# Optimization experiments

Measured on AMD Instinct MI355X. Metric: run time of the kernel, lower is better.

The kernel has to match this reference:

```python
import jax, jax.numpy as jnp
import numpy as np

M = 41
RHO = M / 2.0          # rho=-1 -> M/2
OVERLAPS = 40

def _get_index():
    S = [(n1, n2)
         for n1 in range(-(M // 2), M // 2)
         for n2 in range(-(M // 2), M // 2)
         if abs(n1 * n2) <= RHO * (M // 2)]
    return np.asarray(S, dtype=np.int32)  # [K,2], K=1600 for defaults

_PAIRS = _get_index()


def setup_inputs() -> dict:
    key = jax.random.key(0)
    ks = jax.random.split(key, 7)
    B, L, N = 2, 2048, 2
    K = _PAIRS.shape[0]
    return {
        "x_real": jax.random.normal(ks[0], (B, L, N), jnp.float32),
        "x_imag": jax.random.normal(ks[1], (B, L, N), jnp.float32),
        "task_info": jax.random.uniform(ks[2], (B, 4), jnp.float32),
        "fc_wr": jax.random.normal(ks[3], (K,), jnp.float32) * 0.02,
        "fc_wi": jax.random.normal(ks[4], (K,), jnp.float32) * 0.02,
        "fc_br": jax.random.normal(ks[5], (1,), jnp.float32) * 0.02,
        "fc_bi": jax.random.normal(ks[6], (1,), jnp.float32) * 0.02,
    }


def reference(x_real, x_imag, task_info, fc_wr, fc_wi, fc_br, fc_bi):
    B, L, N = x_real.shape
    x0 = x_real + 1j * x_imag                      # [B,L,N] complex64
    # get_power: dBm -> Watts per mode
    P = 1e-3 * jnp.power(10.0, task_info[:, 0] / 10.0) / N   # [B]

    xf = jnp.fft.fft(x0, axis=1)                   # [B,L,N]
    idx = jnp.arange(L)
    n1 = jnp.asarray(_PAIRS[:, 0])
    n2 = jnp.asarray(_PAIRS[:, 1])

    # torch.roll(x, s, dim=1)[i] == x[(i - s) % L]; vectorize over all K pairs
    def gather(s):                                  # s: [K]
        return xf[:, (idx[:, None] - s[None, :]) % L, :]   # [B,L,K,N]

    A = gather(n1) * jnp.conj(gather(n1 + n2))      # [B,L,K,N]
    E = (A + jnp.roll(A, 1, axis=-1)) * gather(n2)  # [B,L,K,N]

    w = fc_wr + 1j * fc_wi                          # [K]
    b = fc_br[0] + 1j * fc_bi[0]
    delta = jnp.einsum('blkn,k->bln', E, w) + b     # ComplexLinear K->1
    delta = jnp.fft.ifft(delta, axis=1)

    out = (x0 + delta * P[:, None, None])[:, OVERLAPS // 2 : L - OVERLAPS // 2, :]
    # return real/imag stacked so the baseline output is real-valued
    return jnp.stack([out.real, out.imag], axis=-1)  # [B, L-OVERLAPS, N, 2]
```

## Files before the change

### kernel.cpp

```cpp
#include <hip/hip_runtime.h>


#define L_FFT 2048
#define NB 2
#define NM 2
#define ND 40
#define CROP 20
#define LOUT 2008

__device__ __forceinline__ float2 cmul(float2 a, float2 b) {
    return make_float2(a.x*b.x - a.y*b.y, a.x*b.y + a.y*b.x);
}
__device__ __forceinline__ float2 cmulc(float2 a, float2 b) {
    return make_float2(a.x*b.x + a.y*b.y, a.y*b.x - a.x*b.y);
}

template<int SIGN>
__device__ void build_tw(float2* tw, int tid) {
    if (tid < 512) {
        float ang = (float)(SIGN * tid) * 3.0679615757712823e-03f;
        tw[tid] = make_float2(__cosf(ang), __sinf(ang));
    }
}

template<int SIGN>
__device__ float2* fft2048_r4(float2* bufA, float2* bufB, const float2* tw, int tid) {
    float2* src = bufA;
    float2* dst = bufB;
    #pragma unroll
    for (int m = 1; m <= 256; m *= 4) {
        __syncthreads();
        int k2 = tid & (m - 1);
        int jm = tid - k2;
        float2 A = src[tid];
        float2 C = src[tid + 512];
        float2 B = src[tid + 1024];
        float2 D = src[tid + 1536];
        float2 T0 = make_float2(A.x + B.x, A.y + B.y);
        float2 T1 = make_float2(A.x - B.x, A.y - B.y);
        float2 T2 = make_float2(C.x + D.x, C.y + D.y);
        float2 cd = make_float2(C.x - D.x, C.y - D.y);
        float2 T3 = (SIGN < 0) ? make_float2(cd.y, -cd.x)
                               : make_float2(-cd.y, cd.x);
        float2 w1 = tw[jm];
        float2 w2 = cmul(w1, w1);
        float2 w3 = cmul(w2, w1);
        int base = 4 * jm + k2;
        dst[base]         = make_float2(T0.x + T2.x, T0.y + T2.y);
        dst[base + m]     = cmul(make_float2(T1.x + T3.x, T1.y + T3.y), w1);
        dst[base + 2*m]   = cmul(make_float2(T0.x - T2.x, T0.y - T2.y), w2);
        dst[base + 3*m]   = cmul(make_float2(T1.x - T3.x, T1.y - T3.y), w3);
        float2* t = src; src = dst; dst = t;
    }
    __syncthreads();
    #pragma unroll
    for (int it = 0; it < 2; ++it) {
        int q = tid + it * 512;
        float2 a = src[q];
        float2 b = src[q + 1024];
        dst[q]        = make_float2(a.x + b.x, a.y + b.y);
        dst[q + 1024] = make_float2(a.x - b.x, a.y - b.y);
    }
    float2* res = dst;
    __syncthreads();
    return res;
}

__global__ __launch_bounds__(512) void fft_fwd_kernel(const float* __restrict__ xr,
                                                      const float* __restrict__ xi,
                                                      float2* __restrict__ xf,
                                                      float* __restrict__ df) {
    __shared__ float2 bufA[L_FFT];
    __shared__ float2 bufB[L_FFT];
    __shared__ float2 tw[512];
    int bn = blockIdx.x;
    int b = bn >> 1, n = bn & 1;
    int tid = threadIdx.x;
    #pragma unroll
    for (int i = 0; i < 8; ++i)
        df[bn * (L_FFT * 2) + tid + i * 512] = 0.f;
    #pragma unroll
    for (int it = 0; it < 4; ++it) {
        int t = tid + it * 512;
        int gi = (b * L_FFT + t) * NM + n;
        bufA[t] = make_float2(xr[gi], xi[gi]);
    }
    build_tw<-1>(tw, tid);
    float2* res = fft2048_r4<-1>(bufA, bufB, tw, tid);
    #pragma unroll
    for (int it = 0; it < 4; ++it) {
        int f = tid + it * 512;
        xf[bn * L_FFT + f] = res[f];
    }
}

__global__ __launch_bounds__(256) void gs2_kernel(const float2* __restrict__ xf,
                                                  const float* __restrict__ wr,
                                                  const float* __restrict__ wi,
                                                  float* __restrict__ df) {
    __shared__ float2 xs0[336], xs1[336];
    __shared__ float2 Gs[296];
    __shared__ float wrs[40][4], wis[40][4];
    int blk = blockIdx.x;
    int b   = blk / 80;
    int rem = blk % 80;
    int dq  = rem >> 3;
    int l0  = (rem & 7) << 8;
    int tid = threadIdx.x;
    const float2* x0 = xf + (b * 2 + 0) * L_FFT;
    const float2* x1 = xf + (b * 2 + 1) * L_FFT;
    for (int i = tid; i < 336; i += 256) {
        int m = (l0 - 39 + i) & (L_FFT - 1);
        xs0[i] = x0[m];
        xs1[i] = x1[m];
    }
    if (tid < 160) {
        int n1i = tid >> 2, di = tid & 3;
        wrs[n1i][di] = wr[n1i * ND + dq * 4 + di];
        wis[n1i][di] = wi[n1i * ND + dq * 4 + di];
    }
    __syncthreads();
    float2 a0 = make_float2(0.f, 0.f);
    float2 a1 = make_float2(0.f, 0.f);
    #pragma unroll
    for (int di = 0; di < 4; ++di) {
        int d  = dq * 4 + di;
        int dd = d - 20;
        for (int j = tid; j < 295; j += 256) {
            float2 g0 = cmulc(xs0[j + 20], xs0[j + 20 - dd]);
            float2 g1 = cmulc(xs1[j + 20], xs1[j + 20 - dd]);
            Gs[j] = make_float2(g0.x + g1.x, g0.y + g1.y);
        }
        __syncthreads();
        float2 acc = make_float2(0.f, 0.f);
        #pragma unroll
        for (int n1i = 0; n1i < ND; ++n1i) {
            float2 g = Gs[tid + 39 - n1i];
            float wxr = wrs[n1i][di], wxi = wis[n1i][di];
            acc.x += wxr * g.x - wxi * g.y;
            acc.y += wxr * g.y + wxi * g.x;
        }
        int xvi = tid + 39 - dd;
        float2 c0 = cmul(acc, xs0[xvi]);
        float2 c1 = cmul(acc, xs1[xvi]);
        a0.x += c0.x; a0.y += c0.y;
        a1.x += c1.x; a1.y += c1.y;
        __syncthreads();
    }
    int base = (b * 2) * (L_FFT * 2) + (l0 + tid) * 2;
    unsafeAtomicAdd(&df[base + 0], a0.x);
    unsafeAtomicAdd(&df[base + 1], a0.y);
    unsafeAtomicAdd(&df[base + L_FFT * 2 + 0], a1.x);
    unsafeAtomicAdd(&df[base + L_FFT * 2 + 1], a1.y);
}

__global__ __launch_bounds__(512) void ifft_out_kernel(const float* __restrict__ df,
                                                       const float* __restrict__ xr,
                                                       const float* __restrict__ xi,
                                                       const float* __restrict__ task,
                                                       float* __restrict__ out) {
    __shared__ float2 bufA[L_FFT];
    __shared__ float2 bufB[L_FFT];
    __shared__ float2 tw[512];
    int bn = blockIdx.x;
    int b = bn >> 1, n = bn & 1;
    int tid = threadIdx.x;
    const float2* dfreq = (const float2*)df + bn * L_FFT;
    #pragma unroll
    for (int it = 0; it < 4; ++it)
        bufA[tid + it * 512] = dfreq[tid + it * 512];
    build_tw<1>(tw, tid);
    float2* res = fft2048_r4<1>(bufA, bufB, tw, tid);
    float P = 1e-3f * __powf(10.f, task[b * 4] * 0.1f) * 0.5f;
    float scale = P * (1.0f / (float)L_FFT);
    for (int t = CROP + tid; t < L_FFT - CROP; t += 512) {
        int gi = (b * L_FFT + t) * NM + n;
        float2 dv = res[t];
        int oi = ((b * LOUT + (t - CROP)) * NM + n) * 2;
        out[oi]     = xr[gi] + dv.x * scale;
        out[oi + 1] = xi[gi] + dv.y * scale;
    }
}

extern "C" void kernel_launch(void* const* d_in, const int* in_sizes, int n_in,
                              void* d_out, int out_size, void* d_ws, size_t ws_size,
                              hipStream_t stream) {
    const float* xr   = (const float*)d_in[0];
    const float* xi   = (const float*)d_in[1];
    const float* task = (const float*)d_in[2];
    const float* wr   = (const float*)d_in[3];
    const float* wi   = (const float*)d_in[4];
    float* out = (float*)d_out;

    float2* ws = (float2*)d_ws;
    float2* xf = ws;
    float*  df = (float*)(ws + 8192);

    hipLaunchKernelGGL(fft_fwd_kernel,  dim3(NB * NM), dim3(512), 0, stream, xr, xi, xf, df);
    hipLaunchKernelGGL(gs2_kernel,      dim3(160), dim3(256), 0, stream, xf, wr, wi, df);
    hipLaunchKernelGGL(ifft_out_kernel, dim3(NB * NM), dim3(512), 0, stream, df, xr, xi, task, out);
}
```

Baseline: 23.01 us.

## Fuse FFT, correlation and IFFT stages into one kernel with global-counter barriers

Replaces three kernel launches with a single persistent kernel of 80 blocks. Blocks synchronize through agent-scope atomic counters and spin-waits instead of kernel boundaries. The correlation stage now uses 512-thread blocks covering 512 output positions each, where it previously used 160 blocks of 256. The zeroing of df and the counters moves to a hipMemsetAsync. This removes two launch gaps but adds spin-wait overhead, and it relies on all 80 blocks being co-resident.

```diff
diff --git a/kernel.cpp b/kernel.cpp
--- a/kernel.cpp
+++ b/kernel.cpp
@@ -7,12 +7,28 @@
 #define ND 40
 #define CROP 20
 #define LOUT 2008
+#define NBLK 80
+#define NT 512
+#define SLAB 591
+#define GSZ 551
 
 __device__ __forceinline__ float2 cmul(float2 a, float2 b) {
     return make_float2(a.x*b.x - a.y*b.y, a.x*b.y + a.y*b.x);
 }
 __device__ __forceinline__ float2 cmulc(float2 a, float2 b) {
     return make_float2(a.x*b.x + a.y*b.y, a.y*b.x - a.x*b.y);
+}
+
+__device__ __forceinline__ void agent_store(float2* p, float2 v) {
+    __hip_atomic_store((unsigned long long*)p,
+                       __builtin_bit_cast(unsigned long long, v),
+                       __ATOMIC_RELAXED, __HIP_MEMORY_SCOPE_AGENT);
+}
+__device__ __forceinline__ float2 agent_load(const float2* p) {
+    unsigned long long u =
+        __hip_atomic_load((const unsigned long long*)p,
+                          __ATOMIC_RELAXED, __HIP_MEMORY_SCOPE_AGENT);
+    return __builtin_bit_cast(float2, u);
 }
 
 template<int SIGN>
@@ -66,119 +82,132 @@
     return res;
 }
 
-__global__ __launch_bounds__(512) void fft_fwd_kernel(const float* __restrict__ xr,
-                                                      const float* __restrict__ xi,
-                                                      float2* __restrict__ xf,
-                                                      float* __restrict__ df) {
-    __shared__ float2 bufA[L_FFT];
-    __shared__ float2 bufB[L_FFT];
-    __shared__ float2 tw[512];
-    int bn = blockIdx.x;
-    int b = bn >> 1, n = bn & 1;
+__global__ __launch_bounds__(NT) void fused_kernel(const float* __restrict__ xr,
+                                                   const float* __restrict__ xi,
+                                                   const float* __restrict__ task,
+                                                   const float* __restrict__ wr,
+                                                   const float* __restrict__ wi,
+                                                   float* __restrict__ out,
+                                                   float2* __restrict__ xf,
+                                                   float* __restrict__ df,
+                                                   int* __restrict__ cnt) {
+    __shared__ float2 sm[4608];
+    __shared__ float wrs[ND][4], wis[ND][4];
+    int blk = blockIdx.x;
     int tid = threadIdx.x;
-    #pragma unroll
-    for (int i = 0; i < 8; ++i)
-        df[bn * (L_FFT * 2) + tid + i * 512] = 0.f;
-    #pragma unroll
-    for (int it = 0; it < 4; ++it) {
-        int t = tid + it * 512;
-        int gi = (b * L_FFT + t) * NM + n;
-        bufA[t] = make_float2(xr[gi], xi[gi]);
-    }
-    build_tw<-1>(tw, tid);
-    float2* res = fft2048_r4<-1>(bufA, bufB, tw, tid);
-    #pragma unroll
-    for (int it = 0; it < 4; ++it) {
-        int f = tid + it * 512;
-        xf[bn * L_FFT + f] = res[f];
-    }
-}
-
-__global__ __launch_bounds__(256) void gs2_kernel(const float2* __restrict__ xf,
-                                                  const float* __restrict__ wr,
-                                                  const float* __restrict__ wi,
-                                                  float* __restrict__ df) {
-    __shared__ float2 xs0[336], xs1[336];
-    __shared__ float2 Gs[296];
-    __shared__ float wrs[40][4], wis[40][4];
-    int blk = blockIdx.x;
-    int b   = blk / 80;
-    int rem = blk % 80;
-    int dq  = rem >> 3;
-    int l0  = (rem & 7) << 8;
-    int tid = threadIdx.x;
-    const float2* x0 = xf + (b * 2 + 0) * L_FFT;
-    const float2* x1 = xf + (b * 2 + 1) * L_FFT;
-    for (int i = tid; i < 336; i += 256) {
-        int m = (l0 - 39 + i) & (L_FFT - 1);
-        xs0[i] = x0[m];
-        xs1[i] = x1[m];
-    }
-    if (tid < 160) {
-        int n1i = tid >> 2, di = tid & 3;
-        wrs[n1i][di] = wr[n1i * ND + dq * 4 + di];
-        wis[n1i][di] = wi[n1i * ND + dq * 4 + di];
-    }
-    __syncthreads();
-    float2 a0 = make_float2(0.f, 0.f);
-    float2 a1 = make_float2(0.f, 0.f);
-    #pragma unroll
-    for (int di = 0; di < 4; ++di) {
-        int d  = dq * 4 + di;
-        int dd = d - 20;
-        for (int j = tid; j < 295; j += 256) {
-            float2 g0 = cmulc(xs0[j + 20], xs0[j + 20 - dd]);
-            float2 g1 = cmulc(xs1[j + 20], xs1[j + 20 - dd]);
-            Gs[j] = make_float2(g0.x + g1.x, g0.y + g1.y);
-        }
-        __syncthreads();
-        float2 acc = make_float2(0.f, 0.f);
-        #pragma unroll
-        for (int n1i = 0; n1i < ND; ++n1i) {
-            float2 g = Gs[tid + 39 - n1i];
-            float wxr = wrs[n1i][di], wxi = wis[n1i][di];
-            acc.x += wxr * g.x - wxi * g.y;
-            acc.y += wxr * g.y + wxi * g.x;
-        }
-        int xvi = tid + 39 - dd;
-        float2 c0 = cmul(acc, xs0[xvi]);
-        float2 c1 = cmul(acc, xs1[xvi]);
-        a0.x += c0.x; a0.y += c0.y;
-        a1.x += c1.x; a1.y += c1.y;
-        __syncthreads();
-    }
-    int base = (b * 2) * (L_FFT * 2) + (l0 + tid) * 2;
-    unsafeAtomicAdd(&df[base + 0], a0.x);
-    unsafeAtomicAdd(&df[base + 1], a0.y);
-    unsafeAtomicAdd(&df[base + L_FFT * 2 + 0], a1.x);
-    unsafeAtomicAdd(&df[base + L_FFT * 2 + 1], a1.y);
-}
-
-__global__ __launch_bounds__(512) void ifft_out_kernel(const float* __restrict__ df,
-                                                       const float* __restrict__ xr,
-                                                       const float* __restrict__ xi,
-                                                       const float* __restrict__ task,
-                                                       float* __restrict__ out) {
-    __shared__ float2 bufA[L_FFT];
-    __shared__ float2 bufB[L_FFT];
-    __shared__ float2 tw[512];
-    int bn = blockIdx.x;
-    int b = bn >> 1, n = bn & 1;
-    int tid = threadIdx.x;
-    const float2* dfreq = (const float2*)df + bn * L_FFT;
-    #pragma unroll
-    for (int it = 0; it < 4; ++it)
-        bufA[tid + it * 512] = dfreq[tid + it * 512];
-    build_tw<1>(tw, tid);
-    float2* res = fft2048_r4<1>(bufA, bufB, tw, tid);
-    float P = 1e-3f * __powf(10.f, task[b * 4] * 0.1f) * 0.5f;
-    float scale = P * (1.0f / (float)L_FFT);
-    for (int t = CROP + tid; t < L_FFT - CROP; t += 512) {
-        int gi = (b * L_FFT + t) * NM + n;
-        float2 dv = res[t];
-        int oi = ((b * LOUT + (t - CROP)) * NM + n) * 2;
-        out[oi]     = xr[gi] + dv.x * scale;
-        out[oi + 1] = xi[gi] + dv.y * scale;
+    float2* bufA = sm;
+    float2* bufB = sm + 2048;
+    float2* tw   = sm + 4096;
+
+    if (blk < NB * NM) {
+        int b = blk >> 1, n = blk & 1;
+        #pragma unroll
+        for (int it = 0; it < 4; ++it) {
+            int t = tid + it * NT;
+            int gi = (b * L_FFT + t) * NM + n;
+            bufA[t] = make_float2(xr[gi], xi[gi]);
+        }
+        build_tw<-1>(tw, tid);
+        float2* res = fft2048_r4<-1>(bufA, bufB, tw, tid);
+        #pragma unroll
+        for (int it = 0; it < 4; ++it) {
+            int f = tid + it * NT;
+            agent_store(&xf[blk * L_FFT + f], res[f]);
+        }
+        __syncthreads();
+        if (tid == 0)
+            __hip_atomic_fetch_add(&cnt[0], 1, __ATOMIC_RELAXED, __HIP_MEMORY_SCOPE_AGENT);
+    }
+    if (tid == 0)
+        while (__hip_atomic_load(&cnt[0], __ATOMIC_RELAXED, __HIP_MEMORY_SCOPE_AGENT) < NB * NM)
+            __builtin_amdgcn_s_sleep(1);
+    __syncthreads();
+
+    {
+        int b   = blk / 40;
+        int rem = blk % 40;
+        int dq  = rem >> 2;
+        int l0  = (rem & 3) << 9;
+        float2* xs0 = sm;
+        float2* xs1 = sm + SLAB;
+        float2* Gs  = sm + 2 * SLAB;
+        const float2* x0 = xf + (b * 2 + 0) * L_FFT;
+        const float2* x1 = xf + (b * 2 + 1) * L_FFT;
+        for (int i = tid; i < SLAB; i += NT) {
+            int m = (l0 - 39 + i) & (L_FFT - 1);
+            xs0[i] = agent_load(&x0[m]);
+            xs1[i] = agent_load(&x1[m]);
+        }
+        if (tid < 160) {
+            int n1i = tid >> 2, di = tid & 3;
+            wrs[n1i][di] = wr[n1i * ND + dq * 4 + di];
+            wis[n1i][di] = wi[n1i * ND + dq * 4 + di];
+        }
+        __syncthreads();
+        float2 a0 = make_float2(0.f, 0.f);
+        float2 a1 = make_float2(0.f, 0.f);
+        #pragma unroll
+        for (int di = 0; di < 4; ++di) {
+            int d  = dq * 4 + di;
+            int dd = d - 20;
+            for (int j = tid; j < GSZ; j += NT) {
+                float2 g0 = cmulc(xs0[j + 20], xs0[j + 20 - dd]);
+                float2 g1 = cmulc(xs1[j + 20], xs1[j + 20 - dd]);
+                Gs[j] = make_float2(g0.x + g1.x, g0.y + g1.y);
+            }
+            __syncthreads();
+            float2 acc = make_float2(0.f, 0.f);
+            #pragma unroll
+            for (int n1i = 0; n1i < ND; ++n1i) {
+                float2 g = Gs[tid + 39 - n1i];
+                float wxr = wrs[n1i][di], wxi = wis[n1i][di];
+                acc.x += wxr * g.x - wxi * g.y;
+                acc.y += wxr * g.y + wxi * g.x;
+            }
+            int xvi = tid + 39 - dd;
+            float2 c0 = cmul(acc, xs0[xvi]);
+            float2 c1 = cmul(acc, xs1[xvi]);
+            a0.x += c0.x; a0.y += c0.y;
+            a1.x += c1.x; a1.y += c1.y;
+            __syncthreads();
+        }
+        int base = (b * 2) * (L_FFT * 2) + (l0 + tid) * 2;
+        unsafeAtomicAdd(&df[base + 0], a0.x);
+        unsafeAtomicAdd(&df[base + 1], a0.y);
+        unsafeAtomicAdd(&df[base + L_FFT * 2 + 0], a1.x);
+        unsafeAtomicAdd(&df[base + L_FFT * 2 + 1], a1.y);
+        __syncthreads();
+        if (tid == 0) {
+            __threadfence();
+            __hip_atomic_fetch_add(&cnt[32], 1, __ATOMIC_RELAXED, __HIP_MEMORY_SCOPE_AGENT);
+        }
+    }
+    if (blk >= NB * NM) return;
+
+    if (tid == 0)
+        while (__hip_atomic_load(&cnt[32], __ATOMIC_RELAXED, __HIP_MEMORY_SCOPE_AGENT) < NBLK)
+            __builtin_amdgcn_s_sleep(1);
+    __syncthreads();
+
+    {
+        int b = blk >> 1, n = blk & 1;
+        const float2* dfv = (const float2*)df + blk * L_FFT;
+        #pragma unroll
+        for (int it = 0; it < 4; ++it) {
+            int t = tid + it * NT;
+            bufA[t] = agent_load(&dfv[t]);
+        }
+        build_tw<1>(tw, tid);
+        float2* res = fft2048_r4<1>(bufA, bufB, tw, tid);
+        float P = 1e-3f * __powf(10.f, task[b * 4] * 0.1f) * 0.5f;
+        float scale = P * (1.0f / (float)L_FFT);
+        for (int t = CROP + tid; t < L_FFT - CROP; t += NT) {
+            int gi = (b * L_FFT + t) * NM + n;
+            float2 dv = res[t];
+            int oi = ((b * LOUT + (t - CROP)) * NM + n) * 2;
+            out[oi]     = xr[gi] + dv.x * scale;
+            out[oi + 1] = xi[gi] + dv.y * scale;
+        }
     }
 }
 
@@ -193,10 +222,12 @@
     float* out = (float*)d_out;
 
     float2* ws = (float2*)d_ws;
-    float2* xf = ws;
-    float*  df = (float*)(ws + 8192);
-
-    hipLaunchKernelGGL(fft_fwd_kernel,  dim3(NB * NM), dim3(512), 0, stream, xr, xi, xf, df);
-    hipLaunchKernelGGL(gs2_kernel,      dim3(160), dim3(256), 0, stream, xf, wr, wi, df);
-    hipLaunchKernelGGL(ifft_out_kernel, dim3(NB * NM), dim3(512), 0, stream, df, xr, xi, task, out);
-}
+    float2* xf  = ws;
+    float*  df  = (float*)(ws + 8192);
+    int*    cnt = (int*)(df + 16384);
+
+    hipMemsetAsync((void*)df, 0, 16384 * sizeof(float) + 256, stream);
+
+    hipLaunchKernelGGL(fused_kernel, dim3(NBLK), dim3(NT), 0, stream,
+                       xr, xi, task, wr, wi, out, xf, df, cnt);
+}
```

After: 57.52 us. 2.5x slower.

## Fuse forward FFT into the correlation kernel and drop the atomic accumulation

Applied to the files above, without the earlier changes.

The separate forward-FFT kernel is removed. Each of the 64 correlation blocks now computes the 2048-point FFT of both modes for its batch in shared memory, then evaluates all 40 shift offsets for a 64-sample output tile. Partial sums from the eight thread groups are reduced in shared memory and written directly, so the workspace zeroing and float atomics go away. This trades one fewer launch and no global round-trip for redundant FFT work in every block and a much larger shared-memory footprint per block.

```diff
diff --git a/kernel.cpp b/kernel.cpp
--- a/kernel.cpp
+++ b/kernel.cpp
@@ -7,6 +7,10 @@
 #define ND 40
 #define CROP 20
 #define LOUT 2008
+#define NT 512
+#define TILE 64
+#define NGRP 8
+#define GHALO 103
 
 __device__ __forceinline__ float2 cmul(float2 a, float2 b) {
     return make_float2(a.x*b.x - a.y*b.y, a.x*b.y + a.y*b.x);
@@ -24,7 +28,7 @@
 }
 
 template<int SIGN>
-__device__ float2* fft2048_r4(float2* bufA, float2* bufB, const float2* tw, int tid) {
+__device__ void fft2048_r4(float2* bufA, float2* bufB, const float2* tw, int tid) {
     float2* src = bufA;
     float2* dst = bufB;
     #pragma unroll
@@ -61,121 +65,113 @@
         dst[q]        = make_float2(a.x + b.x, a.y + b.y);
         dst[q + 1024] = make_float2(a.x - b.x, a.y - b.y);
     }
-    float2* res = dst;
     __syncthreads();
-    return res;
 }
 
-__global__ __launch_bounds__(512) void fft_fwd_kernel(const float* __restrict__ xr,
+__global__ __launch_bounds__(NT) void gs2_kernel(const float* __restrict__ xr,
+                                                 const float* __restrict__ xi,
+                                                 const float* __restrict__ wr,
+                                                 const float* __restrict__ wi,
+                                                 float2* __restrict__ df) {
+    __shared__ float2 xs0[L_FFT];
+    __shared__ float2 xs1[L_FFT];
+    __shared__ float2 tmp[L_FFT];
+    __shared__ float2 tw[512];
+    __shared__ float  wlr[1600], wli[1600];
+    __shared__ float2 Gs[NGRP][GHALO];
+    __shared__ float2 pr0[NT], pr1[NT];
+
+    int blk = blockIdx.x;
+    int b   = blk >> 5;
+    int l0  = (blk & 31) * TILE;
+    int tid = threadIdx.x;
+
+    for (int t = tid; t < L_FFT; t += NT) {
+        int gi = (b * L_FFT + t) * NM;
+        xs0[t] = make_float2(xr[gi],     xi[gi]);
+        xs1[t] = make_float2(xr[gi + 1], xi[gi + 1]);
+    }
+    for (int i = tid; i < 1600; i += NT) { wlr[i] = wr[i]; wli[i] = wi[i]; }
+    build_tw<-1>(tw, tid);
+
+    fft2048_r4<-1>(xs0, tmp, tw, tid);
+    fft2048_r4<-1>(xs1, tmp, tw, tid);
+
+    int grp = tid >> 6;
+    int lt  = tid & 63;
+    int l   = l0 + lt;
+    float2 acc0 = make_float2(0.f, 0.f);
+    float2 acc1 = make_float2(0.f, 0.f);
+
+    #pragma unroll
+    for (int it = 0; it < 5; ++it) {
+        int d  = it * NGRP + grp;
+        int dd = d - 20;
+        __syncthreads();
+        #pragma unroll
+        for (int p = 0; p < 2; ++p) {
+            int j = lt + p * 64;
+            if (j < GHALO) {
+                int m = l0 - 19 + j;
+                float2 g0 = cmulc(xs0[m & (L_FFT-1)], xs0[(m - dd) & (L_FFT-1)]);
+                float2 g1 = cmulc(xs1[m & (L_FFT-1)], xs1[(m - dd) & (L_FFT-1)]);
+                Gs[grp][j] = make_float2(g0.x + g1.x, g0.y + g1.y);
+            }
+        }
+        __syncthreads();
+        float2 s2 = make_float2(0.f, 0.f);
+        #pragma unroll
+        for (int n1i = 0; n1i < ND; ++n1i) {
+            float2 g = Gs[grp][lt + 39 - n1i];
+            float wxr = wlr[n1i * ND + d], wxi = wli[n1i * ND + d];
+            s2.x += wxr * g.x - wxi * g.y;
+            s2.y += wxr * g.y + wxi * g.x;
+        }
+        float2 xv0 = xs0[(l - dd) & (L_FFT-1)];
+        float2 xv1 = xs1[(l - dd) & (L_FFT-1)];
+        float2 c0 = cmul(s2, xv0);
+        float2 c1 = cmul(s2, xv1);
+        acc0.x += c0.x; acc0.y += c0.y;
+        acc1.x += c1.x; acc1.y += c1.y;
+    }
+    pr0[tid] = acc0;
+    pr1[tid] = acc1;
+    __syncthreads();
+    if (tid < 128) {
+        int n = tid >> 6, lq = tid & 63;
+        float2* pr = n ? pr1 : pr0;
+        float2 s = make_float2(0.f, 0.f);
+        #pragma unroll
+        for (int g = 0; g < NGRP; ++g) {
+            float2 v = pr[g * 64 + lq];
+            s.x += v.x; s.y += v.y;
+        }
+        df[(b * 2 + n) * L_FFT + l0 + lq] = s;
+    }
+}
+
+__global__ __launch_bounds__(NT) void ifft_out_kernel(const float2* __restrict__ df,
+                                                      const float* __restrict__ xr,
                                                       const float* __restrict__ xi,
-                                                      float2* __restrict__ xf,
-                                                      float* __restrict__ df) {
+                                                      const float* __restrict__ task,
+                                                      float* __restrict__ out) {
     __shared__ float2 bufA[L_FFT];
     __shared__ float2 bufB[L_FFT];
     __shared__ float2 tw[512];
     int bn = blockIdx.x;
     int b = bn >> 1, n = bn & 1;
     int tid = threadIdx.x;
-    #pragma unroll
-    for (int i = 0; i < 8; ++i)
-        df[bn * (L_FFT * 2) + tid + i * 512] = 0.f;
-    #pragma unroll
-    for (int it = 0; it < 4; ++it) {
-        int t = tid + it * 512;
-        int gi = (b * L_FFT + t) * NM + n;
-        bufA[t] = make_float2(xr[gi], xi[gi]);
-    }
-    build_tw<-1>(tw, tid);
-    float2* res = fft2048_r4<-1>(bufA, bufB, tw, tid);
-    #pragma unroll
-    for (int it = 0; it < 4; ++it) {
-        int f = tid + it * 512;
-        xf[bn * L_FFT + f] = res[f];
-    }
-}
-
-__global__ __launch_bounds__(256) void gs2_kernel(const float2* __restrict__ xf,
-                                                  const float* __restrict__ wr,
-                                                  const float* __restrict__ wi,
-                                                  float* __restrict__ df) {
-    __shared__ float2 xs0[336], xs1[336];
-    __shared__ float2 Gs[296];
-    __shared__ float wrs[40][4], wis[40][4];
-    int blk = blockIdx.x;
-    int b   = blk / 80;
-    int rem = blk % 80;
-    int dq  = rem >> 3;
-    int l0  = (rem & 7) << 8;
-    int tid = threadIdx.x;
-    const float2* x0 = xf + (b * 2 + 0) * L_FFT;
-    const float2* x1 = xf + (b * 2 + 1) * L_FFT;
-    for (int i = tid; i < 336; i += 256) {
-        int m = (l0 - 39 + i) & (L_FFT - 1);
-        xs0[i] = x0[m];
-        xs1[i] = x1[m];
-    }
-    if (tid < 160) {
-        int n1i = tid >> 2, di = tid & 3;
-        wrs[n1i][di] = wr[n1i * ND + dq * 4 + di];
-        wis[n1i][di] = wi[n1i * ND + dq * 4 + di];
-    }
-    __syncthreads();
-    float2 a0 = make_float2(0.f, 0.f);
-    float2 a1 = make_float2(0.f, 0.f);
-    #pragma unroll
-    for (int di = 0; di < 4; ++di) {
-        int d  = dq * 4 + di;
-        int dd = d - 20;
-        for (int j = tid; j < 295; j += 256) {
-            float2 g0 = cmulc(xs0[j + 20], xs0[j + 20 - dd]);
-            float2 g1 = cmulc(xs1[j + 20], xs1[j + 20 - dd]);
-            Gs[j] = make_float2(g0.x + g1.x, g0.y + g1.y);
-        }
-        __syncthreads();
-        float2 acc = make_float2(0.f, 0.f);
-        #pragma unroll
-        for (int n1i = 0; n1i < ND; ++n1i) {
-            float2 g = Gs[tid + 39 - n1i];
-            float wxr = wrs[n1i][di], wxi = wis[n1i][di];
-            acc.x += wxr * g.x - wxi * g.y;
-            acc.y += wxr * g.y + wxi * g.x;
-        }
-        int xvi = tid + 39 - dd;
-        float2 c0 = cmul(acc, xs0[xvi]);
-        float2 c1 = cmul(acc, xs1[xvi]);
-        a0.x += c0.x; a0.y += c0.y;
-        a1.x += c1.x; a1.y += c1.y;
-        __syncthreads();
-    }
-    int base = (b * 2) * (L_FFT * 2) + (l0 + tid) * 2;
-    unsafeAtomicAdd(&df[base + 0], a0.x);
-    unsafeAtomicAdd(&df[base + 1], a0.y);
-    unsafeAtomicAdd(&df[base + L_FFT * 2 + 0], a1.x);
-    unsafeAtomicAdd(&df[base + L_FFT * 2 + 1], a1.y);
-}
-
-__global__ __launch_bounds__(512) void ifft_out_kernel(const float* __restrict__ df,
-                                                       const float* __restrict__ xr,
-                                                       const float* __restrict__ xi,
-                                                       const float* __restrict__ task,
-                                                       float* __restrict__ out) {
-    __shared__ float2 bufA[L_FFT];
-    __shared__ float2 bufB[L_FFT];
-    __shared__ float2 tw[512];
-    int bn = blockIdx.x;
-    int b = bn >> 1, n = bn & 1;
-    int tid = threadIdx.x;
-    const float2* dfreq = (const float2*)df + bn * L_FFT;
+    const float2* dfreq = df + bn * L_FFT;
     #pragma unroll
     for (int it = 0; it < 4; ++it)
-        bufA[tid + it * 512] = dfreq[tid + it * 512];
+        bufA[tid + it * NT] = dfreq[tid + it * NT];
     build_tw<1>(tw, tid);
-    float2* res = fft2048_r4<1>(bufA, bufB, tw, tid);
+    fft2048_r4<1>(bufA, bufB, tw, tid);
     float P = 1e-3f * __powf(10.f, task[b * 4] * 0.1f) * 0.5f;
     float scale = P * (1.0f / (float)L_FFT);
-    for (int t = CROP + tid; t < L_FFT - CROP; t += 512) {
+    for (int t = CROP + tid; t < L_FFT - CROP; t += NT) {
         int gi = (b * L_FFT + t) * NM + n;
-        float2 dv = res[t];
+        float2 dv = bufA[t];
         int oi = ((b * LOUT + (t - CROP)) * NM + n) * 2;
         out[oi]     = xr[gi] + dv.x * scale;
         out[oi + 1] = xi[gi] + dv.y * scale;
@@ -192,11 +188,8 @@
     const float* wi   = (const float*)d_in[4];
     float* out = (float*)d_out;
 
-    float2* ws = (float2*)d_ws;
-    float2* xf = ws;
-    float*  df = (float*)(ws + 8192);
+    float2* df = (float2*)d_ws;
 
-    hipLaunchKernelGGL(fft_fwd_kernel,  dim3(NB * NM), dim3(512), 0, stream, xr, xi, xf, df);
-    hipLaunchKernelGGL(gs2_kernel,      dim3(160), dim3(256), 0, stream, xf, wr, wi, df);
-    hipLaunchKernelGGL(ifft_out_kernel, dim3(NB * NM), dim3(512), 0, stream, df, xr, xi, task, out);
+    hipLaunchKernelGGL(gs2_kernel,      dim3(64), dim3(NT), 0, stream, xr, xi, wr, wi, df);
+    hipLaunchKernelGGL(ifft_out_kernel, dim3(NB * NM), dim3(NT), 0, stream, df, xr, xi, task, out);
 }
```

Measured after the change: 73.52 us. 219% more time.
